# Kernel tuning notes

Measured on AMD Instinct MI355X. Metric: run time of the kernel, lower is better.

Reference implementation:

```python
import jax, jax.numpy as jnp
from jax import lax
import numpy as np

D_MODEL, D_STATE, D_CONV, EXPAND = 1024, 16, 4, 2
D_INNER = EXPAND * D_MODEL          # 2048
DT_RANK = D_MODEL // 16             # 64
B_SZ, L_SEQ = 2, 2048


def setup_inputs() -> dict:
    key = jax.random.key(0)
    ks = jax.random.split(key, 8)
    x = jax.random.normal(ks[0], (B_SZ, L_SEQ, D_MODEL), jnp.float32)
    inp = {
        "x": x,
        "ln_g": jnp.ones((D_MODEL,), jnp.float32),
        "ln_b": jnp.zeros((D_MODEL,), jnp.float32),
        # fan-in scaled weights for numerical sanity
        "W_in": jax.random.normal(ks[1], (2 * D_INNER, D_MODEL), jnp.float32) / np.sqrt(D_MODEL),
        "conv_w": jax.random.normal(ks[2], (D_INNER, D_CONV), jnp.float32) / np.sqrt(D_CONV),
        "conv_b": jnp.zeros((D_INNER,), jnp.float32),
        "W_xp": jax.random.normal(ks[3], (DT_RANK + 2 * D_STATE, D_INNER), jnp.float32) / np.sqrt(D_INNER),
        "W_dt": jax.random.normal(ks[4], (D_INNER, DT_RANK), jnp.float32) / np.sqrt(DT_RANK),
        "b_dt": jax.random.normal(ks[5], (D_INNER,), jnp.float32) * 0.1 - 4.0,  # softplus(dt) small, like mamba init
        # S4D-real init: A = -exp(A_log), A_log = log(1..d_state)
        "A_log": jnp.broadcast_to(jnp.log(jnp.arange(1, D_STATE + 1, dtype=jnp.float32)), (D_INNER, D_STATE)).copy(),
        "D": jnp.ones((D_INNER,), jnp.float32),
        "W_out": jax.random.normal(ks[6], (D_MODEL, D_INNER), jnp.float32) / np.sqrt(D_INNER),
    }
    return inp


def _selective_scan(u, dt, A, Bm, Cm, Dvec):
    # u, dt: (B, L, d_inner); Bm, Cm: (B, L, d_state); A: (d_inner, d_state)
    def step(h, inputs):
        u_t, dt_t, B_t, C_t = inputs                      # (B,di),(B,di),(B,n),(B,n)
        dA = jnp.exp(dt_t[:, :, None] * A[None])          # (B,di,n), in (0,1) since A<0
        dBu = (dt_t * u_t)[:, :, None] * B_t[:, None, :]  # (B,di,n)
        h = dA * h + dBu
        y = jnp.einsum('bdn,bn->bd', h, C_t)
        return h, y
    xs = (u.transpose(1, 0, 2), dt.transpose(1, 0, 2),
          Bm.transpose(1, 0, 2), Cm.transpose(1, 0, 2))
    h0 = jnp.zeros((u.shape[0], u.shape[2], A.shape[1]), u.dtype)
    _, ys = lax.scan(step, h0, xs)
    return ys.transpose(1, 0, 2) + u * Dvec               # (B, L, d_inner)


def reference(x, ln_g, ln_b, W_in, conv_w, conv_b, W_xp, W_dt, b_dt, A_log, D, W_out):
    d_inner, d_conv = conv_w.shape
    dt_rank = W_dt.shape[1]
    d_state = A_log.shape[1]
    # pre-LayerNorm
    mu = jnp.mean(x, axis=-1, keepdims=True)
    var = jnp.mean(jnp.square(x - mu), axis=-1, keepdims=True)
    xn = (x - mu) * lax.rsqrt(var + 1e-5) * ln_g + ln_b
    # input projection -> (B, L, 2*d_inner)
    xz = jnp.einsum('bld,ed->ble', xn, W_in)
    u, z = jnp.split(xz, 2, axis=-1)
    # causal depthwise conv over time
    u_c = lax.conv_general_dilated(
        u.transpose(0, 2, 1),                 # (B, d_inner, L)
        conv_w[:, None, :],                   # (d_inner, 1, d_conv)
        window_strides=(1,), padding=[(d_conv - 1, 0)],
        feature_group_count=d_inner)
    u_c = jax.nn.silu((u_c + conv_b[None, :, None]).transpose(0, 2, 1))  # (B, L, d_inner)
    # data-dependent dt, B, C
    x_dbl = jnp.einsum('bld,ed->ble', u_c, W_xp)
    dt, Bm, Cm = jnp.split(x_dbl, [dt_rank, dt_rank + d_state], axis=-1)
    dt = jax.nn.softplus(jnp.einsum('blr,dr->bld', dt, W_dt) + b_dt)
    A = -jnp.exp(A_log)
    y = _selective_scan(u_c, dt, A, Bm, Cm, D)
    y = y * jax.nn.silu(z)
    out = jnp.einsum('ble,de->bld', y, W_out)
    return x + out
```

## Files before the change

kernel.cpp:

```cpp
#include <hip/hip_runtime.h>

typedef __bf16 bf16x8 __attribute__((ext_vector_type(8)));
typedef float  f32x4  __attribute__((ext_vector_type(4)));

#define LOG2E 1.44269504088896f

__device__ __forceinline__ float bfl(unsigned short s) {
    return __uint_as_float(((unsigned int)s) << 16);
}
__device__ __forceinline__ unsigned short f2bf(float f) {
    unsigned int x = __float_as_uint(f);
    x += 0x7fffu + ((x >> 16) & 1u);
    return (unsigned short)(x >> 16);
}
__device__ __forceinline__ float fexp2(float x) { return __builtin_amdgcn_exp2f(x); }
__device__ __forceinline__ float fexp(float x)  { return __builtin_amdgcn_exp2f(x * LOG2E); }
__device__ __forceinline__ float frcp(float x)  { return __builtin_amdgcn_rcpf(x); }
__device__ __forceinline__ float silu_f(float x) {
    return x * frcp(1.f + fexp2(-x * LOG2E));
}
__device__ __forceinline__ void gl_lds(const unsigned short* g, unsigned short* l) {
    __builtin_amdgcn_global_load_lds(
        (__attribute__((address_space(1))) const void*)g,
        (__attribute__((address_space(3))) void*)l, 16, 0, 0);
}

#define BSZ   2
#define LSEQ  2048
#define DMODEL 1024
#define DI    2048
#define DS    16
#define NCH   64
#define CL    32

#define WI_N   4194304
#define WXP_N  196608
#define WDT_N  131072
#define WOUT_N 2097152
#define WSEG1  (WI_N)
#define WSEG2  (WI_N + WXP_N)
#define WSEG3  (WI_N + WXP_N + WDT_N)
#define WTOT   (WI_N + WXP_N + WDT_N + WOUT_N)

__global__ __launch_bounds__(256) void cvt_weights(
    const float* __restrict__ w0, const float* __restrict__ w1,
    const float* __restrict__ w2, const float* __restrict__ w3,
    unsigned short* __restrict__ dst)
{
    const size_t e0 = ((size_t)blockIdx.x * 256 + threadIdx.x) * 8;
    if (e0 >= WTOT) return;
    const float* src;
    size_t off;
    if      (e0 < WSEG1) { src = w0; off = e0; }
    else if (e0 < WSEG2) { src = w1; off = e0 - WSEG1; }
    else if (e0 < WSEG3) { src = w2; off = e0 - WSEG2; }
    else                 { src = w3; off = e0 - WSEG3; }
    float4 a = *(const float4*)(src + off);
    float4 b = *(const float4*)(src + off + 4);
    ushort4 lo, hi;
    lo.x = f2bf(a.x); lo.y = f2bf(a.y); lo.z = f2bf(a.z); lo.w = f2bf(a.w);
    hi.x = f2bf(b.x); hi.y = f2bf(b.y); hi.z = f2bf(b.z); hi.w = f2bf(b.w);
    *(ushort4*)(dst + e0) = lo;
    *(ushort4*)(dst + e0 + 4) = hi;
}

__global__ __launch_bounds__(256) void ln_kernel(
    const float* __restrict__ x,
    const float* __restrict__ g,
    const float* __restrict__ b,
    unsigned short* __restrict__ xn)
{
    const int row = blockIdx.x;
    const int tid = threadIdx.x;
    const int lane = tid & 63, wv = tid >> 6;
    const float* xp = x + (size_t)row * DMODEL;

    float4 v = ((const float4*)xp)[tid];
    float s = v.x + v.y + v.z + v.w;
    float q = v.x*v.x + v.y*v.y + v.z*v.z + v.w*v.w;
    #pragma unroll
    for (int o = 32; o > 0; o >>= 1) {
        s += __shfl_down(s, o);
        q += __shfl_down(q, o);
    }
    __shared__ float ss[4], sq[4];
    if (lane == 0) { ss[wv] = s; sq[wv] = q; }
    __syncthreads();
    s = ss[0] + ss[1] + ss[2] + ss[3];
    q = sq[0] + sq[1] + sq[2] + sq[3];
    const float mu  = s * (1.f / DMODEL);
    const float var = q * (1.f / DMODEL) - mu * mu;
    const float rs  = rsqrtf(var + 1e-5f);

    float4 gv = ((const float4*)g)[tid];
    float4 bv = ((const float4*)b)[tid];
    ushort4 o;
    o.x = f2bf((v.x - mu) * rs * gv.x + bv.x);
    o.y = f2bf((v.y - mu) * rs * gv.y + bv.y);
    o.z = f2bf((v.z - mu) * rs * gv.z + bv.z);
    o.w = f2bf((v.w - mu) * rs * gv.w + bv.w);
    ((ushort4*)(xn + (size_t)row * DMODEL))[tid] = o;
}

template<int EPI, int LOGM>
__global__ __launch_bounds__(512, 2) void gemm_pipe256(
    const unsigned short* __restrict__ A,
    const unsigned short* __restrict__ Bw,
    void* __restrict__ Cout,
    const void* __restrict__ aux0,
    int K, int ldc)
{
    __shared__ unsigned short As[2][256 * 64];
    __shared__ unsigned short Bs[2][256 * 64];
    const int tid  = threadIdx.x;
    const int lane = tid & 63;
    const int wid  = tid >> 6;
    const int wm   = (wid >> 2) * 128;
    const int wn   = (wid & 3) * 64;

    const int nwg = gridDim.x;
    const int id  = blockIdx.x;
    const int swz = (id & 7) * (nwg >> 3) + (id >> 3);
    const int bx  = swz & ((1 << LOGM) - 1);
    const int by  = swz >> LOGM;
    const size_t am0 = (size_t)bx * 256;
    const size_t bn0 = (size_t)by * 256;

    const int srow  = lane >> 3;
    const int sslot = (lane & 7) ^ srow;
    const unsigned short* gA = A  + (am0 + wid * 8 + srow) * (size_t)K + sslot * 8;
    const unsigned short* gB = Bw + (bn0 + wid * 8 + srow) * (size_t)K + sslot * 8;

    const int NT = K >> 6;

#define STAGE256(buf, ko)                                                      \
    {   _Pragma("unroll")                                                      \
        for (int j = 0; j < 4; ++j)                                            \
            gl_lds(gA + (size_t)(j * 64) * K + (ko), &As[buf][(j * 64 + wid * 8) * 64]); \
        _Pragma("unroll")                                                      \
        for (int j = 0; j < 4; ++j)                                            \
            gl_lds(gB + (size_t)(j * 64) * K + (ko), &Bs[buf][(j * 64 + wid * 8) * 64]); }

    STAGE256(0, 0)
    STAGE256(1, 64)

    f32x4 acc[8][4];
    f32x4 z4 = {0.f, 0.f, 0.f, 0.f};
    #pragma unroll
    for (int i = 0; i < 8; ++i)
        #pragma unroll
        for (int j = 0; j < 4; ++j) acc[i][j] = z4;

    const int lr  = lane & 15;
    const int lq  = lane >> 4;
    const int key = lr & 7;

#define RD_A(dst, q)                                                           \
    _Pragma("unroll")                                                          \
    for (int i = 0; i < 2; ++i)                                                \
        _Pragma("unroll")                                                      \
        for (int ks = 0; ks < 2; ++ks)                                         \
            dst[i][ks] = *(const bf16x8*)&As[cur][(wm + ((q) * 2 + i) * 16 + lr) * 64 \
                                                  + (((ks * 4 + lq) ^ key) * 8)];

#define MFMA_Q(src, q)                                                         \
    _Pragma("unroll")                                                          \
    for (int i = 0; i < 2; ++i)                                                \
        _Pragma("unroll")                                                      \
        for (int fn = 0; fn < 4; ++fn) {                                       \
            acc[(q) * 2 + i][fn] = __builtin_amdgcn_mfma_f32_16x16x32_bf16(    \
                src[i][0], bfv[fn][0], acc[(q) * 2 + i][fn], 0, 0, 0);         \
            acc[(q) * 2 + i][fn] = __builtin_amdgcn_mfma_f32_16x16x32_bf16(    \
                src[i][1], bfv[fn][1], acc[(q) * 2 + i][fn], 0, 0, 0);         }

    for (int t = 0; t < NT; ++t) {
        const int cur = t & 1;
        if (t < NT - 1) asm volatile("s_waitcnt vmcnt(8)" ::: "memory");
        else            asm volatile("s_waitcnt vmcnt(0)" ::: "memory");
        __builtin_amdgcn_s_barrier();
        __builtin_amdgcn_sched_barrier(0);

        bf16x8 bfv[4][2], fA[2][2], fB[2][2];
        #pragma unroll
        for (int fn = 0; fn < 4; ++fn)
            #pragma unroll
            for (int ks = 0; ks < 2; ++ks)
                bfv[fn][ks] = *(const bf16x8*)&Bs[cur][(wn + fn * 16 + lr) * 64
                                                        + (((ks * 4 + lq) ^ key) * 8)];
        RD_A(fA, 0)
        asm volatile("s_waitcnt lgkmcnt(0)" ::: "memory");
        __builtin_amdgcn_sched_barrier(0);

        RD_A(fB, 1)
        __builtin_amdgcn_s_setprio(1);
        MFMA_Q(fA, 0)
        __builtin_amdgcn_s_setprio(0);
        asm volatile("s_waitcnt lgkmcnt(0)" ::: "memory");
        __builtin_amdgcn_sched_barrier(0);

        RD_A(fA, 2)
        __builtin_amdgcn_s_setprio(1);
        MFMA_Q(fB, 1)
        __builtin_amdgcn_s_setprio(0);
        asm volatile("s_waitcnt lgkmcnt(0)" ::: "memory");
        __builtin_amdgcn_sched_barrier(0);

        RD_A(fB, 3)
        __builtin_amdgcn_s_setprio(1);
        MFMA_Q(fA, 2)
        __builtin_amdgcn_s_setprio(0);
        asm volatile("s_waitcnt lgkmcnt(0)" ::: "memory");
        __builtin_amdgcn_sched_barrier(0);

        __builtin_amdgcn_s_barrier();
        if (t + 2 < NT) {
            STAGE256(cur, (size_t)(t + 2) * 64)
        }
        __builtin_amdgcn_s_setprio(1);
        MFMA_Q(fB, 3)
        __builtin_amdgcn_s_setprio(0);
    }
#undef RD_A
#undef MFMA_Q
#undef STAGE256

    const int er = lq * 4;
    const int ec = lr;
    #pragma unroll
    for (int fm = 0; fm < 8; ++fm) {
        #pragma unroll
        for (int fn = 0; fn < 4; ++fn) {
            const size_t col = bn0 + wn + fn * 16 + ec;
            #pragma unroll
            for (int r = 0; r < 4; ++r) {
                const size_t row = am0 + wm + fm * 16 + er + r;
                float v = acc[fm][fn][r];
                if constexpr (EPI == 0) {
                    ((unsigned short*)Cout)[row * ldc + col] = f2bf(v);
                } else {
                    float t2 = v + ((const float*)aux0)[row * ldc + col];
                    ((float*)Cout)[row * ldc + col] = t2;
                }
            }
        }
    }
}

template<int EPI, int LOGNB>
__global__ __launch_bounds__(512, 2) void gemm_pipe128(
    const unsigned short* __restrict__ A,
    const unsigned short* __restrict__ Bw,
    void* __restrict__ Cout,
    const void* __restrict__ aux0,
    int K, int ldc)
{
    __shared__ unsigned short As[2][128 * 64];
    __shared__ unsigned short Bs[2][128 * 64];
    const int tid  = threadIdx.x;
    const int lane = tid & 63;
    const int wid  = tid >> 6;
    const int wm   = (wid >> 2) * 64;
    const int wn   = (wid & 3) * 32;

    const int nwg = gridDim.x;
    const int id  = blockIdx.x;
    const int swz = (id & 7) * (nwg >> 3) + (id >> 3);
    const int bn_i = swz & ((1 << LOGNB) - 1);
    const int bm_i = swz >> LOGNB;
    const size_t am0 = (size_t)bm_i * 128;
    const size_t bn0 = (size_t)bn_i * 128;

    const int srow  = lane >> 3;
    const int sslot = (lane & 7) ^ srow;
    const unsigned short* gA = A  + (am0 + wid * 16 + srow) * (size_t)K + sslot * 8;
    const unsigned short* gB = Bw + (bn0 + wid * 16 + srow) * (size_t)K + sslot * 8;

    const int NT = K >> 6;

#define STAGE128(buf, ko)                                                      \
    {   _Pragma("unroll")                                                      \
        for (int j = 0; j < 2; ++j)                                            \
            gl_lds(gA + (size_t)(j * 8) * K + (ko), &As[buf][(wid * 16 + j * 8) * 64]); \
        _Pragma("unroll")                                                      \
        for (int j = 0; j < 2; ++j)                                            \
            gl_lds(gB + (size_t)(j * 8) * K + (ko), &Bs[buf][(wid * 16 + j * 8) * 64]); }

    STAGE128(0, 0)
    STAGE128(1, 64)

    f32x4 acc[4][2];
    f32x4 z4 = {0.f, 0.f, 0.f, 0.f};
    #pragma unroll
    for (int i = 0; i < 4; ++i) { acc[i][0] = z4; acc[i][1] = z4; }

    const int lr  = lane & 15;
    const int lq  = lane >> 4;
    const int key = lr & 7;

#define RD_A128(dst, h)                                                        \
    _Pragma("unroll")                                                          \
    for (int i = 0; i < 2; ++i)                                                \
        _Pragma("unroll")                                                      \
        for (int ks = 0; ks < 2; ++ks)                                         \
            dst[i][ks] = *(const bf16x8*)&As[cur][(wm + ((h) * 2 + i) * 16 + lr) * 64 \
                                                  + (((ks * 4 + lq) ^ key) * 8)];

#define MFMA_H(src, h)                                                         \
    _Pragma("unroll")                                                          \
    for (int i = 0; i < 2; ++i)                                                \
        _Pragma("unroll")                                                      \
        for (int fn = 0; fn < 2; ++fn) {                                       \
            acc[(h) * 2 + i][fn] = __builtin_amdgcn_mfma_f32_16x16x32_bf16(    \
                src[i][0], bfv[fn][0], acc[(h) * 2 + i][fn], 0, 0, 0);         \
            acc[(h) * 2 + i][fn] = __builtin_amdgcn_mfma_f32_16x16x32_bf16(    \
                src[i][1], bfv[fn][1], acc[(h) * 2 + i][fn], 0, 0, 0);         }

    for (int t = 0; t < NT; ++t) {
        const int cur = t & 1;
        if (t < NT - 1) asm volatile("s_waitcnt vmcnt(4)" ::: "memory");
        else            asm volatile("s_waitcnt vmcnt(0)" ::: "memory");
        __builtin_amdgcn_s_barrier();
        __builtin_amdgcn_sched_barrier(0);

        bf16x8 bfv[2][2], fA[2][2], fB[2][2];
        #pragma unroll
        for (int fn = 0; fn < 2; ++fn)
            #pragma unroll
            for (int ks = 0; ks < 2; ++ks)
                bfv[fn][ks] = *(const bf16x8*)&Bs[cur][(wn + fn * 16 + lr) * 64
                                                        + (((ks * 4 + lq) ^ key) * 8)];
        RD_A128(fA, 0)
        asm volatile("s_waitcnt lgkmcnt(0)" ::: "memory");
        __builtin_amdgcn_sched_barrier(0);

        RD_A128(fB, 1)
        __builtin_amdgcn_s_setprio(1);
        MFMA_H(fA, 0)
        __builtin_amdgcn_s_setprio(0);
        asm volatile("s_waitcnt lgkmcnt(0)" ::: "memory");
        __builtin_amdgcn_sched_barrier(0);

        __builtin_amdgcn_s_barrier();
        if (t + 2 < NT) {
            STAGE128(cur, (size_t)(t + 2) * 64)
        }
        __builtin_amdgcn_s_setprio(1);
        MFMA_H(fB, 1)
        __builtin_amdgcn_s_setprio(0);
    }
#undef RD_A128
#undef MFMA_H
#undef STAGE128

    const int er = lq * 4;
    const int ec = lr;
    #pragma unroll
    for (int fm = 0; fm < 4; ++fm) {
        #pragma unroll
        for (int fn = 0; fn < 2; ++fn) {
            const size_t col = bn0 + wn + fn * 16 + ec;
            #pragma unroll
            for (int r = 0; r < 4; ++r) {
                const size_t row = am0 + wm + fm * 16 + er + r;
                float v = acc[fm][fn][r];
                if constexpr (EPI == 0) {
                    ((unsigned short*)Cout)[row * ldc + col] = f2bf(v);
                } else {
                    float t2 = v + ((const float*)aux0)[row * ldc + col];
                    ((float*)Cout)[row * ldc + col] = t2;
                }
            }
        }
    }
}

template<int BM, int BN, int EPI, int LOG_NBXM>
__global__ __launch_bounds__(256) void gemm_lds(
    const unsigned short* __restrict__ A,
    const unsigned short* __restrict__ Bw,
    void* __restrict__ Cout,
    const void* __restrict__ aux0,
    int K, int ldc)
{
    constexpr int FM = BM / 32;
    constexpr int FN = BN / 32;
    __shared__ unsigned short As[BM * 64];
    __shared__ unsigned short Bs[BN * 64];
    const int tid  = threadIdx.x;
    const int lane = tid & 63;
    const int wv   = tid >> 6;
    const int wm   = (wv >> 1) * (BM / 2);
    const int wn   = (wv & 1)  * (BN / 2);

    const int nwg = gridDim.x;
    const int id  = blockIdx.x;
    const int swz = (id & 7) * (nwg >> 3) + (id >> 3);
    const int bx  = swz & ((1 << LOG_NBXM) - 1);
    const int by  = swz >> LOG_NBXM;

    f32x4 acc[FM][FN];
    f32x4 z4 = {0.f, 0.f, 0.f, 0.f};
    #pragma unroll
    for (int i = 0; i < FM; ++i)
        #pragma unroll
        for (int j = 0; j < FN; ++j) acc[i][j] = z4;

    const size_t am0 = (size_t)bx * BM;
    const size_t bn0 = (size_t)by * BN;
    const int srow  = lane >> 3;
    const int scol  = (lane & 7) * 8;

    for (int k0 = 0; k0 < K; k0 += 64) {
        __syncthreads();
        #pragma unroll
        for (int i = 0; i < BM / 32; ++i) {
            const int rb = (wv * (BM / 32) + i) * 8;
            gl_lds(&A[(am0 + rb + srow) * (size_t)K + k0 + scol], &As[rb * 64]);
        }
        #pragma unroll
        for (int i = 0; i < BN / 32; ++i) {
            const int rb = (wv * (BN / 32) + i) * 8;
            gl_lds(&Bw[(bn0 + rb + srow) * (size_t)K + k0 + scol], &Bs[rb * 64]);
        }
        __syncthreads();
        const int lr = lane & 15, lk = (lane >> 4) * 8;
        #pragma unroll
        for (int ks = 0; ks < 2; ++ks) {
            bf16x8 af[FM], bfv[FN];
            #pragma unroll
            for (int fm = 0; fm < FM; ++fm)
                af[fm] = *(const bf16x8*)&As[(wm + fm * 16 + lr) * 64 + ks * 32 + lk];
            #pragma unroll
            for (int fn = 0; fn < FN; ++fn)
                bfv[fn] = *(const bf16x8*)&Bs[(wn + fn * 16 + lr) * 64 + ks * 32 + lk];
            #pragma unroll
            for (int fm = 0; fm < FM; ++fm)
                #pragma unroll
                for (int fn = 0; fn < FN; ++fn)
                    acc[fm][fn] = __builtin_amdgcn_mfma_f32_16x16x32_bf16(
                        af[fm], bfv[fn], acc[fm][fn], 0, 0, 0);
        }
    }

    const int er = (lane >> 4) * 4;
    const int ec = lane & 15;
    #pragma unroll
    for (int fm = 0; fm < FM; ++fm) {
        #pragma unroll
        for (int fn = 0; fn < FN; ++fn) {
            const size_t col = bn0 + wn + fn * 16 + ec;
            #pragma unroll
            for (int r = 0; r < 4; ++r) {
                const size_t row = am0 + wm + fm * 16 + er + r;
                float v = acc[fm][fn][r];
                if constexpr (EPI == 0) {
                    ((unsigned short*)Cout)[row * ldc + col] = f2bf(v);
                } else if constexpr (EPI == 2) {
                    float t = v + ((const float*)aux0)[col];
                    float e = fexp2(t * LOG2E);
                    float sp = 0.69314718056f * __builtin_amdgcn_logf(1.f + e);
                    if (t > 20.f) sp = t;
                    ((unsigned short*)Cout)[row * ldc + col] = f2bf(sp);
                } else {
                    float t = v + ((const float*)aux0)[row * ldc + col];
                    ((float*)Cout)[row * ldc + col] = t;
                }
            }
        }
    }
}

__global__ __launch_bounds__(256) void gemm4_splitk(
    const unsigned short* __restrict__ A,
    const unsigned short* __restrict__ Bw,
    float* __restrict__ Cpart)
{
    constexpr int LDP = 72;
    __shared__ unsigned short As[64 * LDP];
    __shared__ unsigned short Bs[96 * LDP];
    const int tid  = threadIdx.x;
    const int lane = tid & 63;
    const int wv   = tid >> 6;
    const int wm   = (wv >> 1) * 32;
    const int wn   = (wv & 1)  * 48;

    f32x4 acc[2][3];
    f32x4 z4 = {0.f, 0.f, 0.f, 0.f};
    #pragma unroll
    for (int i = 0; i < 2; ++i)
        #pragma unroll
        for (int j = 0; j < 3; ++j) acc[i][j] = z4;

    const size_t am0 = (size_t)blockIdx.x * 64;
    const int kz = blockIdx.y;
    const int kbeg = kz * 256;
    const int r0 = tid >> 3;
    const int c0 = (tid & 7) * 8;

    for (int k0 = kbeg; k0 < kbeg + 256; k0 += 64) {
        __syncthreads();
        #pragma unroll
        for (int p = 0; p < 2; ++p) {
            int r = r0 + p * 32;
            *(uint4*)&As[r * LDP + c0] = *(const uint4*)&A[(am0 + r) * (size_t)2048 + k0 + c0];
        }
        #pragma unroll
        for (int p = 0; p < 3; ++p) {
            int r = r0 + p * 32;
            *(uint4*)&Bs[r * LDP + c0] = *(const uint4*)&Bw[(size_t)r * 2048 + k0 + c0];
        }
        __syncthreads();
        const int lr = lane & 15, lk = (lane >> 4) * 8;
        #pragma unroll
        for (int ks = 0; ks < 2; ++ks) {
            bf16x8 af[2], bfv[3];
            #pragma unroll
            for (int fm = 0; fm < 2; ++fm)
                af[fm] = *(const bf16x8*)&As[(wm + fm * 16 + lr) * LDP + ks * 32 + lk];
            #pragma unroll
            for (int fn = 0; fn < 3; ++fn)
                bfv[fn] = *(const bf16x8*)&Bs[(wn + fn * 16 + lr) * LDP + ks * 32 + lk];
            #pragma unroll
            for (int fm = 0; fm < 2; ++fm)
                #pragma unroll
                for (int fn = 0; fn < 3; ++fn)
                    acc[fm][fn] = __builtin_amdgcn_mfma_f32_16x16x32_bf16(
                        af[fm], bfv[fn], acc[fm][fn], 0, 0, 0);
        }
    }

    const int er = (lane >> 4) * 4;
    const int ec = lane & 15;
    float* out = Cpart + (size_t)kz * 4096 * 96;
    #pragma unroll
    for (int fm = 0; fm < 2; ++fm) {
        #pragma unroll
        for (int fn = 0; fn < 3; ++fn) {
            const int col = wn + fn * 16 + ec;
            #pragma unroll
            for (int r = 0; r < 4; ++r) {
                const size_t row = am0 + wm + fm * 16 + er + r;
                out[row * 96 + col] = acc[fm][fn][r];
            }
        }
    }
}

__global__ __launch_bounds__(256) void reduce_xdbl(
    const float* __restrict__ Cpart,
    float* __restrict__ x_dbl,
    unsigned short* __restrict__ dtlow)
{
    const int e = blockIdx.x * 256 + threadIdx.x;
    float s = 0.f;
    #pragma unroll
    for (int kz = 0; kz < 8; ++kz) s += Cpart[(size_t)kz * 393216 + e];
    x_dbl[e] = s;
    const int row = e / 96, col = e - row * 96;
    if (col < 64) dtlow[row * 64 + col] = f2bf(s);
}

__global__ __launch_bounds__(256) void conv_silu(
    const unsigned short* __restrict__ xz,
    const float* __restrict__ convw,
    const float* __restrict__ convb,
    unsigned short* __restrict__ u_c)
{
    const size_t i = (size_t)blockIdx.x * 256 + threadIdx.x;
    if (i >= (size_t)BSZ * LSEQ * DI) return;
    const int d = (int)(i & (DI - 1));
    const size_t bl = i >> 11;
    const int l = (int)(bl & (LSEQ - 1));
    const int b = (int)(bl >> 11);

    float4 wv = *(const float4*)&convw[d * 4];
    float acc = convb[d];
    const size_t rowbase = (size_t)(b * LSEQ) * (2 * DI) + d;
    if (l >= 3) acc += bfl(xz[rowbase + (size_t)(l - 3) * (2 * DI)]) * wv.x;
    if (l >= 2) acc += bfl(xz[rowbase + (size_t)(l - 2) * (2 * DI)]) * wv.y;
    if (l >= 1) acc += bfl(xz[rowbase + (size_t)(l - 1) * (2 * DI)]) * wv.z;
    acc += bfl(xz[rowbase + (size_t)l * (2 * DI)]) * wv.w;
    u_c[i] = f2bf(silu_f(acc));
}

__device__ __forceinline__ bool load_A(const float* __restrict__ A_log, int d, float* An2) {
    bool fast = true;
    #pragma unroll
    for (int i = 0; i < 4; ++i) {
        float4 a = *(const float4*)&A_log[(size_t)d * DS + i * 4];
        float e0 = fexp(a.x), e1 = fexp(a.y), e2 = fexp(a.z), e3 = fexp(a.w);
        fast = fast && fabsf(e0 - (4*i+1)) < 1e-3f * (4*i+1)
                    && fabsf(e1 - (4*i+2)) < 1e-3f * (4*i+2)
                    && fabsf(e2 - (4*i+3)) < 1e-3f * (4*i+3)
                    && fabsf(e3 - (4*i+4)) < 1e-3f * (4*i+4);
        An2[4*i+0] = -e0 * LOG2E; An2[4*i+1] = -e1 * LOG2E;
        An2[4*i+2] = -e2 * LOG2E; An2[4*i+3] = -e3 * LOG2E;
    }
    return fast;
}

__global__ __launch_bounds__(256) void scan1(
    const unsigned short* __restrict__ dt,
    const unsigned short* __restrict__ u_c,
    const float* __restrict__ x_dbl,
    const float* __restrict__ A_log,
    float* __restrict__ chunk_h,
    float* __restrict__ Ssum)
{
    const int d = blockIdx.x * 256 + threadIdx.x;
    const int b = blockIdx.y, c = blockIdx.z;
    const int tid = threadIdx.x;

    __shared__ float sB[CL][DS];
    if (tid < 128) {
        int s = tid >> 2, j = (tid & 3) * 4;
        *(float4*)&sB[s][j] =
            *(const float4*)&x_dbl[(size_t)(b * LSEQ + c * CL + s) * 96 + 64 + j];
    }

    float An2[DS];
    const bool fast = load_A(A_log, d, An2);
    __syncthreads();

    float h[DS];
    #pragma unroll
    for (int n = 0; n < DS; ++n) h[n] = 0.f;
    float S = 0.f;
    const size_t base = (size_t)(b * LSEQ + c * CL) * DI + d;
    if (fast) {
        for (int s = 0; s < CL; ++s) {
            float dtt = bfl(dt[base + (size_t)s * DI]);
            float ut  = bfl(u_c[base + (size_t)s * DI]);
            S += dtt;
            float dtu = dtt * ut;
            float e1 = fexp2(-dtt * LOG2E);
            float p = 1.f;
            #pragma unroll
            for (int n = 0; n < DS; ++n) {
                p *= e1;
                h[n] = p * h[n] + dtu * sB[s][n];
            }
        }
    } else {
        for (int s = 0; s < CL; ++s) {
            float dtt = bfl(dt[base + (size_t)s * DI]);
            float ut  = bfl(u_c[base + (size_t)s * DI]);
            S += dtt;
            float dtu = dtt * ut;
            #pragma unroll
            for (int n = 0; n < DS; ++n) {
                float dA = fexp2(dtt * An2[n]);
                h[n] = dA * h[n] + dtu * sB[s][n];
            }
        }
    }
    const size_t co = ((size_t)((b * NCH + c) * DI) + d) * DS;
    #pragma unroll
    for (int n = 0; n < DS; ++n) chunk_h[co + n] = h[n];
    Ssum[(size_t)(b * NCH + c) * DI + d] = S;
}

__global__ __launch_bounds__(256) void scan2(
    float* __restrict__ chunk_h,
    const float* __restrict__ Ssum,
    const float* __restrict__ A_log)
{
    const int gid = blockIdx.x * 256 + threadIdx.x;
    const int b = gid >> 15;
    const int rem = gid & 32767;
    const int d = rem >> 4;
    const int n = rem & 15;
    const float A2 = -fexp(A_log[(size_t)d * DS + n]) * LOG2E;
    float H = 0.f;
    for (int c = 0; c < NCH; ++c) {
        const size_t idx = ((size_t)((b * NCH + c) * DI) + d) * DS + n;
        float hl = chunk_h[idx];
        float S  = Ssum[(size_t)(b * NCH + c) * DI + d];
        chunk_h[idx] = H;
        H = fexp2(A2 * S) * H + hl;
    }
}

__global__ __launch_bounds__(256) void scan3(
    const unsigned short* __restrict__ dt,
    const unsigned short* __restrict__ u_c,
    const float* __restrict__ x_dbl,
    const float* __restrict__ A_log,
    const float* __restrict__ Hstart,
    const float* __restrict__ Dvec,
    const unsigned short* __restrict__ xz,
    unsigned short* __restrict__ yb)
{
    const int d = blockIdx.x * 256 + threadIdx.x;
    const int b = blockIdx.y, c = blockIdx.z;
    const int tid = threadIdx.x;

    __shared__ float sBC[CL][32];
    {
        int s = tid >> 3, j = (tid & 7) * 4;
        *(float4*)&sBC[s][j] =
            *(const float4*)&x_dbl[(size_t)(b * LSEQ + c * CL + s) * 96 + 64 + j];
    }

    float An2[DS];
    const bool fast = load_A(A_log, d, An2);
    const float Dd = Dvec[d];
    float h[DS];
    const size_t co = ((size_t)((b * NCH + c) * DI) + d) * DS;
    #pragma unroll
    for (int n = 0; n < DS; ++n) h[n] = Hstart[co + n];
    __syncthreads();

    const size_t base  = (size_t)(b * LSEQ + c * CL) * DI + d;
    const size_t zbase = (size_t)(b * LSEQ + c * CL) * (2 * DI) + DI + d;
    if (fast) {
        for (int s = 0; s < CL; ++s) {
            float dtt = bfl(dt[base + (size_t)s * DI]);
            float ut  = bfl(u_c[base + (size_t)s * DI]);
            float dtu = dtt * ut;
            float e1 = fexp2(-dtt * LOG2E);
            float p = 1.f;
            float a0 = 0.f, a1 = 0.f;
            #pragma unroll
            for (int n = 0; n < DS; ++n) {
                p *= e1;
                h[n] = p * h[n] + dtu * sBC[s][n];
                if (n & 1) a1 += h[n] * sBC[s][16 + n];
                else       a0 += h[n] * sBC[s][16 + n];
            }
            float y = a0 + a1 + Dd * ut;
            float z = bfl(xz[zbase + (size_t)s * (2 * DI)]);
            yb[base + (size_t)s * DI] = f2bf(y * silu_f(z));
        }
    } else {
        for (int s = 0; s < CL; ++s) {
            float dtt = bfl(dt[base + (size_t)s * DI]);
            float ut  = bfl(u_c[base + (size_t)s * DI]);
            float dtu = dtt * ut;
            float a0 = 0.f, a1 = 0.f;
            #pragma unroll
            for (int n = 0; n < DS; ++n) {
                float dA = fexp2(dtt * An2[n]);
                h[n] = dA * h[n] + dtu * sBC[s][n];
                if (n & 1) a1 += h[n] * sBC[s][16 + n];
                else       a0 += h[n] * sBC[s][16 + n];
            }
            float y = a0 + a1 + Dd * ut;
            float z = bfl(xz[zbase + (size_t)s * (2 * DI)]);
            yb[base + (size_t)s * DI] = f2bf(y * silu_f(z));
        }
    }
}

extern "C" void kernel_launch(void* const* d_in, const int* in_sizes, int n_in,
                              void* d_out, int out_size, void* d_ws, size_t ws_size,
                              hipStream_t stream) {
    const float* x      = (const float*)d_in[0];
    const float* ln_g   = (const float*)d_in[1];
    const float* ln_b   = (const float*)d_in[2];
    const float* W_in   = (const float*)d_in[3];
    const float* conv_w = (const float*)d_in[4];
    const float* conv_b = (const float*)d_in[5];
    const float* W_xp   = (const float*)d_in[6];
    const float* W_dt   = (const float*)d_in[7];
    const float* b_dt   = (const float*)d_in[8];
    const float* A_log  = (const float*)d_in[9];
    const float* Dv     = (const float*)d_in[10];
    const float* W_out  = (const float*)d_in[11];
    float* out = (float*)d_out;

    char* w = (char*)d_ws;
    unsigned short* xn     = (unsigned short*)(w + 0);
    unsigned short* xz     = (unsigned short*)(w + 8388608);
    unsigned short* u_c    = (unsigned short*)(w + 41943040);
    float*          x_dbl  = (float*)         (w + 58720256);
    unsigned short* dtlow  = (unsigned short*)(w + 60293120);
    unsigned short* dtb    = (unsigned short*)(w + 60817408);
    float*          chunkh = (float*)         (w + 77594624);
    float*          Ssum   = (float*)         (w + 94371840);
    unsigned short* yb     = (unsigned short*)(w + 95420416);
    unsigned short* wbf    = (unsigned short*)(w + 112197632);
    float*          Cpart  = (float*)         (w + 125435904);
    unsigned short* Wi_bf   = wbf;
    unsigned short* Wxp_bf  = wbf + WSEG1;
    unsigned short* Wdt_bf  = wbf + WSEG2;
    unsigned short* Wout_bf = wbf + WSEG3;
    (void)in_sizes; (void)n_in; (void)out_size; (void)ws_size;

    const int MROWS = BSZ * LSEQ;

    cvt_weights<<<(WTOT / 8 + 255) / 256, 256, 0, stream>>>(
        W_in, W_xp, W_dt, W_out, wbf);
    ln_kernel<<<MROWS, 256, 0, stream>>>(x, ln_g, ln_b, xn);
    gemm_pipe256<0, 4><<<256, 512, 0, stream>>>(
        xn, Wi_bf, xz, nullptr, DMODEL, 2 * DI);
    conv_silu<<<(MROWS * DI) / 256, 256, 0, stream>>>(xz, conv_w, conv_b, u_c);
    gemm4_splitk<<<dim3(64, 8), 256, 0, stream>>>(u_c, Wxp_bf, Cpart);
    reduce_xdbl<<<(MROWS * 96) / 256, 256, 0, stream>>>(Cpart, x_dbl, dtlow);
    gemm_lds<128, 64, 2, 5><<<1024, 256, 0, stream>>>(
        dtlow, Wdt_bf, dtb, b_dt, 64, DI);
    scan1<<<dim3(DI / 256, BSZ, NCH), 256, 0, stream>>>(
        dtb, u_c, x_dbl, A_log, chunkh, Ssum);
    scan2<<<(BSZ * DI * DS) / 256, 256, 0, stream>>>(chunkh, Ssum, A_log);
    scan3<<<dim3(DI / 256, BSZ, NCH), 256, 0, stream>>>(
        dtb, u_c, x_dbl, A_log, chunkh, Dv, xz, yb);
    gemm_pipe128<3, 3><<<256, 512, 0, stream>>>(
        yb, Wout_bf, out, x, DI, DMODEL);
}
```

Measured before the change: 182.4 us.

## Restructure in-projection GEMM into eight-phase interleaved load/MFMA pipeline

Replaces the two-stage double-buffered main loop of the 256x256 input-projection GEMM with an eight-phase schedule. Each phase issues a quarter of the next tile's global-to-LDS loads, split into A and B pieces, interleaved with a quarter of the MFMA work, separated by barriers. The aim is to spread memory traffic evenly across the compute and hide load latency, in the style of hipBLASLt-like 8-wave ping-pong kernels. It adds more barriers per K-step and depends on fragile vmcnt accounting; only one of the pipeline's five GEMMs changes.

```diff
diff --git a/kernel.cpp b/kernel.cpp
--- a/kernel.cpp
+++ b/kernel.cpp
@@ -103,7 +103,7 @@
 }
 
 template<int EPI, int LOGM>
-__global__ __launch_bounds__(512, 2) void gemm_pipe256(
+__global__ __launch_bounds__(512, 2) void gemm_8ph(
     const unsigned short* __restrict__ A,
     const unsigned short* __restrict__ Bw,
     void* __restrict__ Cout,
@@ -132,17 +132,15 @@
     const unsigned short* gB = Bw + (bn0 + wid * 8 + srow) * (size_t)K + sslot * 8;
 
     const int NT = K >> 6;
-
-#define STAGE256(buf, ko)                                                      \
-    {   _Pragma("unroll")                                                      \
-        for (int j = 0; j < 4; ++j)                                            \
-            gl_lds(gA + (size_t)(j * 64) * K + (ko), &As[buf][(j * 64 + wid * 8) * 64]); \
-        _Pragma("unroll")                                                      \
-        for (int j = 0; j < 4; ++j)                                            \
-            gl_lds(gB + (size_t)(j * 64) * K + (ko), &Bs[buf][(j * 64 + wid * 8) * 64]); }
-
-    STAGE256(0, 0)
-    STAGE256(1, 64)
+    const int NI = NT >> 1;
+
+#define STA(b, j, ko) gl_lds(gA + (size_t)((j) * 64) * K + (ko), &As[b][((j) * 64 + wid * 8) * 64]);
+#define STB(b, j, ko) gl_lds(gB + (size_t)((j) * 64) * K + (ko), &Bs[b][((j) * 64 + wid * 8) * 64]);
+
+    STA(0, 0, 0) STA(0, 1, 0) STA(0, 2, 0) STA(0, 3, 0)
+    STB(0, 0, 0) STB(0, 1, 0) STB(0, 2, 0) STB(0, 3, 0)
+    STB(1, 0, 64) STB(1, 1, 64) STB(1, 2, 64) STB(1, 3, 64)
+    STA(1, 0, 64) STA(1, 2, 64)
 
     f32x4 acc[8][4];
     f32x4 z4 = {0.f, 0.f, 0.f, 0.f};
@@ -155,74 +153,99 @@
     const int lq  = lane >> 4;
     const int key = lr & 7;
 
-#define RD_A(dst, q)                                                           \
+    asm volatile("s_waitcnt vmcnt(6)" ::: "memory");
+    __builtin_amdgcn_s_barrier();
+
+    bf16x8 bfv[4][2], fA[2][2];
+
+#define RD_B(b)                                                                \
     _Pragma("unroll")                                                          \
-    for (int i = 0; i < 2; ++i)                                                \
+    for (int fn = 0; fn < 4; ++fn)                                             \
         _Pragma("unroll")                                                      \
         for (int ks = 0; ks < 2; ++ks)                                         \
-            dst[i][ks] = *(const bf16x8*)&As[cur][(wm + ((q) * 2 + i) * 16 + lr) * 64 \
-                                                  + (((ks * 4 + lq) ^ key) * 8)];
-
-#define MFMA_Q(src, q)                                                         \
+            bfv[fn][ks] = *(const bf16x8*)&Bs[b][(wn + fn * 16 + lr) * 64      \
+                                                 + (((ks * 4 + lq) ^ key) * 8)];
+
+#define RD_AQ(b, q)                                                            \
     _Pragma("unroll")                                                          \
-    for (int i = 0; i < 2; ++i)                                                \
+    for (int i2 = 0; i2 < 2; ++i2)                                             \
+        _Pragma("unroll")                                                      \
+        for (int ks = 0; ks < 2; ++ks)                                         \
+            fA[i2][ks] = *(const bf16x8*)&As[b][(wm + (q) * 32 + i2 * 16 + lr) * 64 \
+                                                + (((ks * 4 + lq) ^ key) * 8)];
+
+#define MFMA16(q)                                                              \
+    _Pragma("unroll")                                                          \
+    for (int i2 = 0; i2 < 2; ++i2)                                             \
         _Pragma("unroll")                                                      \
         for (int fn = 0; fn < 4; ++fn) {                                       \
-            acc[(q) * 2 + i][fn] = __builtin_amdgcn_mfma_f32_16x16x32_bf16(    \
-                src[i][0], bfv[fn][0], acc[(q) * 2 + i][fn], 0, 0, 0);         \
-            acc[(q) * 2 + i][fn] = __builtin_amdgcn_mfma_f32_16x16x32_bf16(    \
-                src[i][1], bfv[fn][1], acc[(q) * 2 + i][fn], 0, 0, 0);         }
-
-    for (int t = 0; t < NT; ++t) {
-        const int cur = t & 1;
-        if (t < NT - 1) asm volatile("s_waitcnt vmcnt(8)" ::: "memory");
-        else            asm volatile("s_waitcnt vmcnt(0)" ::: "memory");
-        __builtin_amdgcn_s_barrier();
-        __builtin_amdgcn_sched_barrier(0);
-
-        bf16x8 bfv[4][2], fA[2][2], fB[2][2];
-        #pragma unroll
-        for (int fn = 0; fn < 4; ++fn)
-            #pragma unroll
-            for (int ks = 0; ks < 2; ++ks)
-                bfv[fn][ks] = *(const bf16x8*)&Bs[cur][(wn + fn * 16 + lr) * 64
-                                                        + (((ks * 4 + lq) ^ key) * 8)];
-        RD_A(fA, 0)
-        asm volatile("s_waitcnt lgkmcnt(0)" ::: "memory");
-        __builtin_amdgcn_sched_barrier(0);
-
-        RD_A(fB, 1)
-        __builtin_amdgcn_s_setprio(1);
-        MFMA_Q(fA, 0)
-        __builtin_amdgcn_s_setprio(0);
-        asm volatile("s_waitcnt lgkmcnt(0)" ::: "memory");
-        __builtin_amdgcn_sched_barrier(0);
-
-        RD_A(fA, 2)
-        __builtin_amdgcn_s_setprio(1);
-        MFMA_Q(fB, 1)
-        __builtin_amdgcn_s_setprio(0);
-        asm volatile("s_waitcnt lgkmcnt(0)" ::: "memory");
-        __builtin_amdgcn_sched_barrier(0);
-
-        RD_A(fB, 3)
-        __builtin_amdgcn_s_setprio(1);
-        MFMA_Q(fA, 2)
-        __builtin_amdgcn_s_setprio(0);
-        asm volatile("s_waitcnt lgkmcnt(0)" ::: "memory");
-        __builtin_amdgcn_sched_barrier(0);
-
-        __builtin_amdgcn_s_barrier();
-        if (t + 2 < NT) {
-            STAGE256(cur, (size_t)(t + 2) * 64)
-        }
-        __builtin_amdgcn_s_setprio(1);
-        MFMA_Q(fB, 3)
-        __builtin_amdgcn_s_setprio(0);
-    }
-#undef RD_A
-#undef MFMA_Q
-#undef STAGE256
+            acc[(q) * 2 + i2][fn] = __builtin_amdgcn_mfma_f32_16x16x32_bf16(   \
+                fA[i2][0], bfv[fn][0], acc[(q) * 2 + i2][fn], 0, 0, 0);        \
+            acc[(q) * 2 + i2][fn] = __builtin_amdgcn_mfma_f32_16x16x32_bf16(   \
+                fA[i2][1], bfv[fn][1], acc[(q) * 2 + i2][fn], 0, 0, 0);        }
+
+#define PH_SYNC                                                                \
+    __builtin_amdgcn_s_barrier();                                              \
+    asm volatile("s_waitcnt lgkmcnt(0)" ::: "memory");                         \
+    __builtin_amdgcn_sched_barrier(0);
+
+    for (int i = 0; i < NI; ++i) {
+        const bool last = (i == NI - 1);
+        const size_t ko1 = (size_t)(2 * i + 1) * 64;
+        const size_t ko2 = ko1 + 64;
+        const size_t ko3 = ko1 + 128;
+
+        RD_AQ(0, 0) RD_B(0)
+        STA(1, 1, ko1) STA(1, 3, ko1)
+        PH_SYNC
+        __builtin_amdgcn_s_setprio(1); MFMA16(0) __builtin_amdgcn_s_setprio(0);
+        __builtin_amdgcn_s_barrier();
+        RD_AQ(0, 1)
+        if (!last) { STB(0, 0, ko2) STB(0, 1, ko2) }
+        PH_SYNC
+        __builtin_amdgcn_s_setprio(1); MFMA16(1) __builtin_amdgcn_s_setprio(0);
+        __builtin_amdgcn_s_barrier();
+        RD_AQ(0, 2)
+        if (!last) { STB(0, 2, ko2) STB(0, 3, ko2) }
+        PH_SYNC
+        __builtin_amdgcn_s_setprio(1); MFMA16(2) __builtin_amdgcn_s_setprio(0);
+        __builtin_amdgcn_s_barrier();
+        RD_AQ(0, 3)
+        if (!last) { STA(0, 0, ko2) STA(0, 2, ko2) }
+        PH_SYNC
+        __builtin_amdgcn_s_setprio(1); MFMA16(3) __builtin_amdgcn_s_setprio(0);
+        if (last) asm volatile("s_waitcnt vmcnt(0)" ::: "memory");
+        else      asm volatile("s_waitcnt vmcnt(6)" ::: "memory");
+        __builtin_amdgcn_s_barrier();
+        RD_AQ(1, 0) RD_B(1)
+        if (!last) { STA(0, 1, ko2) STA(0, 3, ko2) }
+        PH_SYNC
+        __builtin_amdgcn_s_setprio(1); MFMA16(0) __builtin_amdgcn_s_setprio(0);
+        __builtin_amdgcn_s_barrier();
+        RD_AQ(1, 1)
+        if (!last) { STB(1, 0, ko3) STB(1, 1, ko3) }
+        PH_SYNC
+        __builtin_amdgcn_s_setprio(1); MFMA16(1) __builtin_amdgcn_s_setprio(0);
+        __builtin_amdgcn_s_barrier();
+        RD_AQ(1, 2)
+        if (!last) { STB(1, 2, ko3) STB(1, 3, ko3) }
+        PH_SYNC
+        __builtin_amdgcn_s_setprio(1); MFMA16(2) __builtin_amdgcn_s_setprio(0);
+        __builtin_amdgcn_s_barrier();
+        RD_AQ(1, 3)
+        if (!last) { STA(1, 0, ko3) STA(1, 2, ko3) }
+        PH_SYNC
+        __builtin_amdgcn_s_setprio(1); MFMA16(3) __builtin_amdgcn_s_setprio(0);
+        if (!last) asm volatile("s_waitcnt vmcnt(6)" ::: "memory");
+        __builtin_amdgcn_s_barrier();
+    }
+    asm volatile("s_waitcnt vmcnt(0)" ::: "memory");
+#undef STA
+#undef STB
+#undef RD_B
+#undef RD_AQ
+#undef MFMA16
+#undef PH_SYNC
 
     const int er = lq * 4;
     const int ec = lr;
@@ -792,7 +815,7 @@
     cvt_weights<<<(WTOT / 8 + 255) / 256, 256, 0, stream>>>(
         W_in, W_xp, W_dt, W_out, wbf);
     ln_kernel<<<MROWS, 256, 0, stream>>>(x, ln_g, ln_b, xn);
-    gemm_pipe256<0, 4><<<256, 512, 0, stream>>>(
+    gemm_8ph<0, 4><<<256, 512, 0, stream>>>(
         xn, Wi_bf, xz, nullptr, DMODEL, 2 * DI);
     conv_silu<<<(MROWS * DI) / 256, 256, 0, stream>>>(xz, conv_w, conv_b, u_c);
     gemm4_splitk<<<dim3(64, 8), 256, 0, stream>>>(u_c, Wxp_bf, Cpart);
```

Result: no change. 182.6 us (+0.1%).
